# Kernel optimization log

Measured on AMD Instinct MI355X. Metric: run time of the kernel, lower is better.

## Reference

```python
import jax, jax.numpy as jnp
import numpy as np

P, L, E, D, NL, FF = 1024, 32, 512, 768, 6, 3072
H_PA, H_TR = 4, 8
VOCAB = 256


def layer_norm(x, w, b, eps=1e-5):
    mu = x.mean(-1, keepdims=True)
    var = ((x - mu) ** 2).mean(-1, keepdims=True)
    return (x - mu) / jnp.sqrt(var + eps) * w + b


def mha(x, wqkv, bqkv, wo, bo, nheads, key_mask=None):
    # x: [B,S,E]; torch nn.MultiheadAttention semantics (scale q by 1/sqrt(d))
    B, S, Emb = x.shape
    d = Emb // nheads
    qkv = x @ wqkv.T + bqkv
    q, k, v = jnp.split(qkv, 3, axis=-1)
    hd = lambda t: t.reshape(B, S, nheads, d).transpose(0, 2, 1, 3)
    q, k, v = hd(q) * (d ** -0.5), hd(k), hd(v)
    scores = jnp.einsum('bhqd,bhkd->bhqk', q, k)
    if key_mask is not None:
        scores = jnp.where(key_mask[:, None, None, :], scores, -1e9)
    a = jax.nn.softmax(scores, axis=-1)
    o = jnp.einsum('bhqk,bhkd->bhqd', a, v).transpose(0, 2, 1, 3).reshape(B, S, Emb)
    return o @ wo.T + bo


def setup_inputs() -> dict:
    key = jax.random.key(0)
    ks = jax.random.split(key, 32)
    n = lambda i, shape, s=0.02: (jax.random.normal(ks[i], shape, dtype=jnp.float32) * s)
    x = lambda i, shape: jax.random.normal(ks[i], shape, dtype=jnp.float32) * (1.0 / np.sqrt(shape[-1]))
    tokens = jax.random.randint(ks[0], (P, L), 0, VOCAB, dtype=jnp.int32)
    lengths = jax.random.randint(ks[1], (P,), 4, L + 1, dtype=jnp.int32)
    byte_emb = n(2, (VOCAB, E)).at[0].set(0.0)  # padding_idx=0
    inp = {
        'tokens': tokens, 'lengths': lengths,
        'byte_emb': byte_emb,
        'local_pos_emb': n(3, (L, E)),
        'patch_pos_emb': n(4, (P, D)),
        'pa_qkv_w': x(5, (3 * E, E)), 'pa_qkv_b': jnp.zeros((3 * E,), jnp.float32),
        'pa_out_w': x(6, (E, E)), 'pa_out_b': jnp.zeros((E,), jnp.float32),
        'proj_w': x(7, (D, E)), 'proj_b': jnp.zeros((D,), jnp.float32),
        'layers_qkv_w': x(8, (NL, 3 * D, D)), 'layers_qkv_b': jnp.zeros((NL, 3 * D), jnp.float32),
        'layers_out_w': x(9, (NL, D, D)), 'layers_out_b': jnp.zeros((NL, D), jnp.float32),
        'layers_ln1_w': jnp.ones((NL, D), jnp.float32), 'layers_ln1_b': jnp.zeros((NL, D), jnp.float32),
        'layers_ln2_w': jnp.ones((NL, D), jnp.float32), 'layers_ln2_b': jnp.zeros((NL, D), jnp.float32),
        'layers_ff1_w': x(10, (NL, FF, D)), 'layers_ff1_b': jnp.zeros((NL, FF), jnp.float32),
        'layers_ff2_w': x(11, (NL, D, FF)), 'layers_ff2_b': jnp.zeros((NL, D), jnp.float32),
        'ln_f_w': jnp.ones((D,), jnp.float32), 'ln_f_b': jnp.zeros((D,), jnp.float32),
    }
    return inp


def reference(tokens, lengths, byte_emb, local_pos_emb, patch_pos_emb,
              pa_qkv_w, pa_qkv_b, pa_out_w, pa_out_b, proj_w, proj_b,
              layers_qkv_w, layers_qkv_b, layers_out_w, layers_out_b,
              layers_ln1_w, layers_ln1_b, layers_ln2_w, layers_ln2_b,
              layers_ff1_w, layers_ff1_b, layers_ff2_w, layers_ff2_b,
              ln_f_w, ln_f_b):
    mask = jnp.arange(L) < lengths[:, None]  # [P,L] valid-byte mask
    # encode_patches: byte embed + local positions, zero padded slots
    emb = byte_emb[tokens] + local_pos_emb[None, :, :]  # [P,L,E]
    emb = emb * mask[..., None].astype(emb.dtype)
    # per-patch MHA over bytes (key padding mask), vectorized across patches
    attn = mha(emb, pa_qkv_w, pa_qkv_b, pa_out_w, pa_out_b, H_PA, key_mask=mask)
    cnt = mask.sum(-1, keepdims=True).astype(emb.dtype)
    patch_repr = (attn * mask[..., None].astype(emb.dtype)).sum(1) / cnt  # [P,E] masked mean
    # project to hidden and add patch-level positions
    h = patch_repr @ proj_w.T + proj_b + patch_pos_emb[:P]
    h = h[None]  # [1,P,D]
    # pre-norm transformer encoder, gelu FFN
    for i in range(NL):
        hn = layer_norm(h, layers_ln1_w[i], layers_ln1_b[i])
        h = h + mha(hn, layers_qkv_w[i], layers_qkv_b[i], layers_out_w[i], layers_out_b[i], H_TR)
        hn = layer_norm(h, layers_ln2_w[i], layers_ln2_b[i])
        ff = jax.nn.gelu(hn @ layers_ff1_w[i].T + layers_ff1_b[i], approximate=False)
        h = h + ff @ layers_ff2_w[i].T + layers_ff2_b[i]
    return layer_norm(h, ln_f_w, ln_f_b)[0]  # [P,D]
```

## Files before the change

kernel.cpp:

```cpp
#include <hip/hip_runtime.h>
#include <hip/hip_bf16.h>
#include <math.h>

typedef __hip_bfloat16 bf16;
typedef unsigned short u16;
typedef __attribute__((ext_vector_type(8))) short short8;
typedef __attribute__((ext_vector_type(4))) float f32x4;

#define PP 1024
#define LL 32
#define EE 512
#define DD 768
#define NLAYER 6
#define FFDIM 3072

__device__ __forceinline__ float bf2f(u16 u) { return __uint_as_float(((unsigned)u) << 16); }
__device__ __forceinline__ u16 f2b(float x) {
  unsigned u = __float_as_uint(x);
  return (u16)((u + 0x7FFFu + ((u >> 16) & 1u)) >> 16);
}

__global__ __launch_bounds__(256) void cvt4(
    const float* s0, const float* s1, const float* s2, const float* s3,
    u16* d0, u16* d1, u16* d2, u16* d3,
    int n0, int n1, int n2, int n3)
{
  int r = blockIdx.y;
  const float* s = r == 0 ? s0 : r == 1 ? s1 : r == 2 ? s2 : s3;
  u16* d        = r == 0 ? d0 : r == 1 ? d1 : r == 2 ? d2 : d3;
  int n4        = r == 0 ? n0 : r == 1 ? n1 : r == 2 ? n2 : n3;
  int i = blockIdx.x * 256 + threadIdx.x;
  if (i < n4) {
    float4 v = ((const float4*)s)[i];
    ushort4 o;
    o.x = f2b(v.x); o.y = f2b(v.y); o.z = f2b(v.z); o.w = f2b(v.w);
    ((ushort4*)d)[i] = o;
  }
}

__global__ __launch_bounds__(256) void embed_table(
    const float* __restrict__ be, const float* __restrict__ lp, bf16* __restrict__ T)
{
  int i = blockIdx.x * 256 + threadIdx.x;
  int r = i >> 6, c = (i & 63) << 3;
  int t = r >> 5, l = r & 31;
  const float* bp = be + ((long)t << 9) + c;
  const float* pp = lp + ((long)l << 9) + c;
  float4 x0 = *(const float4*)bp, x1 = *(const float4*)(bp + 4);
  float4 y0 = *(const float4*)pp, y1 = *(const float4*)(pp + 4);
  short8 o;
  o[0] = (short)f2b(x0.x + y0.x); o[1] = (short)f2b(x0.y + y0.y);
  o[2] = (short)f2b(x0.z + y0.z); o[3] = (short)f2b(x0.w + y0.w);
  o[4] = (short)f2b(x1.x + y1.x); o[5] = (short)f2b(x1.y + y1.y);
  o[6] = (short)f2b(x1.z + y1.z); o[7] = (short)f2b(x1.w + y1.w);
  *(short8*)((u16*)T + ((long)r << 9) + c) = o;
}

template<bool AEMB>
__global__ __launch_bounds__(256) void gemm64(
    const bf16* A, long sAb, int lda,
    const bf16* B, long sBb, int ldb,
    float* Cf, bf16* Cb, long sCb, int ldc,
    const float* bias, int biasStride,
    const float* addf,
    int M, int N, int K, int act,
    const int* tokens, const int* lengths,
    const float* be, const float* lp)
{
  __shared__ u16 As[2][64][72];
  __shared__ u16 Bs[2][64][72];
  const int bz = blockIdx.z;
  const u16* Ap = (const u16*)A + (long)bz * sAb;
  const u16* Bp = (const u16*)B + (long)bz * sBb;
  const long coff = (long)bz * sCb;
  const int m0 = blockIdx.x << 6, n0 = blockIdx.y << 6;
  const int tid = threadIdx.x;
  const int wave = tid >> 6, lane = tid & 63;
  const int sr = tid >> 3;
  const int scc = (tid & 7) << 3;
  const int br0 = n0 + sr, br1 = n0 + sr + 32;
  const short8 zz = {0,0,0,0,0,0,0,0};
  f32x4 acc[4] = {{0.f,0.f,0.f,0.f},{0.f,0.f,0.f,0.f},{0.f,0.f,0.f,0.f},{0.f,0.f,0.f,0.f}};

#define LOADA(row, kk, dest)                                                   \
  do {                                                                         \
    if (!AEMB) {                                                               \
      dest = *(const short8*)(Ap + (long)(row) * lda + (kk));                  \
    } else {                                                                   \
      int rr = (row); int ll = rr & 31;                                        \
      if (ll < lengths[rr >> 5]) {                                             \
        const float* bpp = be + ((long)tokens[rr] << 9) + (kk);                \
        const float* lpp = lp + ((long)ll << 9) + (kk);                        \
        float4 x0 = *(const float4*)bpp, x1 = *(const float4*)(bpp + 4);       \
        float4 y0 = *(const float4*)lpp, y1 = *(const float4*)(lpp + 4);       \
        dest[0] = (short)f2b(x0.x + y0.x); dest[1] = (short)f2b(x0.y + y0.y);  \
        dest[2] = (short)f2b(x0.z + y0.z); dest[3] = (short)f2b(x0.w + y0.w);  \
        dest[4] = (short)f2b(x1.x + y1.x); dest[5] = (short)f2b(x1.y + y1.y);  \
        dest[6] = (short)f2b(x1.z + y1.z); dest[7] = (short)f2b(x1.w + y1.w);  \
      } else dest = zz;                                                        \
    }                                                                          \
  } while (0)

  {
    int ch = K < 64 ? K : 64;
    bool kv = scc < ch;
    short8 a0 = zz, a1 = zz, b0 = zz, b1 = zz;
    if (kv) {
      LOADA(m0 + sr, scc, a0);
      LOADA(m0 + sr + 32, scc, a1);
      if (br0 < N) b0 = *(const short8*)(Bp + (long)br0 * ldb + scc);
      if (br1 < N) b1 = *(const short8*)(Bp + (long)br1 * ldb + scc);
    }
    *(short8*)&As[0][sr][scc] = a0;
    *(short8*)&As[0][sr + 32][scc] = a1;
    *(short8*)&Bs[0][sr][scc] = b0;
    *(short8*)&Bs[0][sr + 32][scc] = b1;
  }
  __syncthreads();

  const int arow = (wave << 4) + (lane & 15);
  const int kq = (lane >> 4) << 3;
  int buf = 0;
  for (int k0 = 0; k0 < K; k0 += 64) {
    int knext = k0 + 64;
    bool more = knext < K;
    short8 a0 = zz, a1 = zz, b0 = zz, b1 = zz;
    if (more) {
      int ch = K - knext; if (ch > 64) ch = 64;
      bool kv = scc < ch;
      if (kv) {
        LOADA(m0 + sr, knext + scc, a0);
        LOADA(m0 + sr + 32, knext + scc, a1);
        if (br0 < N) b0 = *(const short8*)(Bp + (long)br0 * ldb + knext + scc);
        if (br1 < N) b1 = *(const short8*)(Bp + (long)br1 * ldb + knext + scc);
      }
    }
    int rem = K - k0; if (rem > 64) rem = 64;
    {
      short8 af = *(const short8*)&As[buf][arow][kq];
#pragma unroll
      for (int nt = 0; nt < 4; nt++) {
        short8 bfr = *(const short8*)&Bs[buf][(nt << 4) + (lane & 15)][kq];
        acc[nt] = __builtin_amdgcn_mfma_f32_16x16x32_bf16(af, bfr, acc[nt], 0, 0, 0);
      }
    }
    if (rem > 32) {
      short8 af = *(const short8*)&As[buf][arow][32 + kq];
#pragma unroll
      for (int nt = 0; nt < 4; nt++) {
        short8 bfr = *(const short8*)&Bs[buf][(nt << 4) + (lane & 15)][32 + kq];
        acc[nt] = __builtin_amdgcn_mfma_f32_16x16x32_bf16(af, bfr, acc[nt], 0, 0, 0);
      }
    }
    if (more) {
      int nb = buf ^ 1;
      *(short8*)&As[nb][sr][scc] = a0;
      *(short8*)&As[nb][sr + 32][scc] = a1;
      *(short8*)&Bs[nb][sr][scc] = b0;
      *(short8*)&Bs[nb][sr + 32][scc] = b1;
      __syncthreads();
      buf = nb;
    }
  }
#undef LOADA

  int rbase = m0 + (wave << 4) + ((lane >> 4) << 2);
#pragma unroll
  for (int nt = 0; nt < 4; nt++) {
    int c = n0 + (nt << 4) + (lane & 15);
    if (c >= N) continue;
    float bvl = bias ? bias[bz * biasStride + c] : 0.f;
#pragma unroll
    for (int j = 0; j < 4; j++) {
      int r = rbase + j;
      long idx = coff + (long)r * ldc + c;
      float v = acc[nt][j] + bvl;
      if (addf) v += addf[idx];
      if (act == 1) v = 0.5f * v * (1.f + erff(v * 0.70710678118654752f));
      if (Cf) Cf[idx] = v;
      if (Cb) Cb[idx] = __float2bfloat16(v);
    }
  }
}

__global__ __launch_bounds__(256) void patch_attn(
    const bf16* __restrict__ qkt,
    const int* __restrict__ tokens, const int* __restrict__ lengths,
    const float* __restrict__ byte_emb, const float* __restrict__ local_pos,
    bf16* __restrict__ Z)
{
  __shared__ float wsum[4][32];
  __shared__ int tok_s[32];
  __shared__ int cnt_s;
  int p = blockIdx.x;
  int tid = threadIdx.x;
  if (tid < 32) tok_s[tid] = tokens[p * 32 + tid];
  if (tid == 0) cnt_s = lengths[p];
  __syncthreads();
  int cnt = cnt_s;
  int h = tid >> 6, lane = tid & 63;
  const int rsel = lane & 15;
  const int ksel = (lane >> 4) << 3;
  const u16* qkb = (const u16*)qkt + h * 128;
  const long r0 = ((long)((tok_s[rsel] << 5) | rsel)) << 10;
  const long r1 = ((long)((tok_s[16 + rsel] << 5) | (16 + rsel))) << 10;

  f32x4 acc[2][2] = {{{0.f,0.f,0.f,0.f},{0.f,0.f,0.f,0.f}},
                     {{0.f,0.f,0.f,0.f},{0.f,0.f,0.f,0.f}}};
#pragma unroll
  for (int kc = 0; kc < 4; kc++) {
    int ko = kc * 32 + ksel;
    short8 a0 = *(const short8*)(qkb + r0 + ko);
    short8 a1 = *(const short8*)(qkb + r1 + ko);
    short8 b0 = *(const short8*)(qkb + r0 + 512 + ko);
    short8 b1 = *(const short8*)(qkb + r1 + 512 + ko);
    acc[0][0] = __builtin_amdgcn_mfma_f32_16x16x32_bf16(a0, b0, acc[0][0], 0, 0, 0);
    acc[0][1] = __builtin_amdgcn_mfma_f32_16x16x32_bf16(a0, b1, acc[0][1], 0, 0, 0);
    acc[1][0] = __builtin_amdgcn_mfma_f32_16x16x32_bf16(a1, b0, acc[1][0], 0, 0, 0);
    acc[1][1] = __builtin_amdgcn_mfma_f32_16x16x32_bf16(a1, b1, acc[1][1], 0, 0, 0);
  }

  const float scale = 0.088388347648318447f;
  int j0 = lane & 15, j1 = 16 + j0;
  bool v0 = j0 < cnt, v1 = j1 < cnt;
  int rowq = (lane >> 4) << 2;
  float cs0 = 0.f, cs1 = 0.f;
#pragma unroll
  for (int ti = 0; ti < 2; ti++) {
    float s0[4], s1[4], mx[4], sm[4], e0[4], e1[4];
#pragma unroll
    for (int r = 0; r < 4; r++) {
      s0[r] = acc[ti][0][r] * scale;
      s1[r] = acc[ti][1][r] * scale;
      float a = v0 ? s0[r] : -1e30f;
      float b = v1 ? s1[r] : -1e30f;
      mx[r] = fmaxf(a, b);
    }
#pragma unroll
    for (int d = 1; d < 16; d <<= 1)
#pragma unroll
      for (int r = 0; r < 4; r++) mx[r] = fmaxf(mx[r], __shfl_xor(mx[r], d));
#pragma unroll
    for (int r = 0; r < 4; r++) {
      e0[r] = v0 ? __expf(s0[r] - mx[r]) : 0.f;
      e1[r] = v1 ? __expf(s1[r] - mx[r]) : 0.f;
      sm[r] = e0[r] + e1[r];
    }
#pragma unroll
    for (int d = 1; d < 16; d <<= 1)
#pragma unroll
      for (int r = 0; r < 4; r++) sm[r] += __shfl_xor(sm[r], d);
#pragma unroll
    for (int r = 0; r < 4; r++) {
      int row = ti * 16 + rowq + r;
      if (row < cnt) {
        float inv = 1.f / sm[r];
        cs0 += e0[r] * inv;
        cs1 += e1[r] * inv;
      }
    }
  }
  cs0 += __shfl_xor(cs0, 16); cs0 += __shfl_xor(cs0, 32);
  cs1 += __shfl_xor(cs1, 16); cs1 += __shfl_xor(cs1, 32);
  if (lane < 16) {
    float invc = 1.f / (float)cnt;
    wsum[h][lane] = cs0 * invc;
    wsum[h][16 + lane] = cs1 * invc;
  }
  __syncthreads();

  for (int e = tid; e < 512; e += 256) {
    float za0 = 0.f, za1 = 0.f, za2 = 0.f, za3 = 0.f;
    for (int j = 0; j < cnt; j++) {
      float ev = byte_emb[((long)tok_s[j] << 9) + e] + local_pos[((long)j << 9) + e];
      za0 += wsum[0][j] * ev;
      za1 += wsum[1][j] * ev;
      za2 += wsum[2][j] * ev;
      za3 += wsum[3][j] * ev;
    }
    long zb = (long)p * 2048;
    Z[zb + e]        = __float2bfloat16(za0);
    Z[zb + 512 + e]  = __float2bfloat16(za1);
    Z[zb + 1024 + e] = __float2bfloat16(za2);
    Z[zb + 1536 + e] = __float2bfloat16(za3);
  }
}

__global__ __launch_bounds__(256) void ln_kernel(
    const float* __restrict__ x, const float* __restrict__ w, const float* __restrict__ b,
    bf16* outb, float* outf, int N)
{
  __shared__ float red[8];
  __shared__ float mv[2];
  int row = blockIdx.x;
  const float* xr = x + (long)row * N;
  int tid = threadIdx.x, lane = tid & 63, wave = tid >> 6;
  float s = 0.f, s2 = 0.f;
  for (int c = tid; c < N; c += 256) { float v = xr[c]; s += v; s2 += v * v; }
  for (int o = 32; o; o >>= 1) { s += __shfl_down(s, o); s2 += __shfl_down(s2, o); }
  if (lane == 0) { red[wave] = s; red[4 + wave] = s2; }
  __syncthreads();
  if (tid == 0) {
    float ts = red[0] + red[1] + red[2] + red[3];
    float ts2 = red[4] + red[5] + red[6] + red[7];
    float mu = ts / N;
    float var = ts2 / N - mu * mu;
    mv[0] = mu; mv[1] = rsqrtf(var + 1e-5f);
  }
  __syncthreads();
  float mu = mv[0], rstd = mv[1];
  for (int c = tid; c < N; c += 256) {
    float v = (xr[c] - mu) * rstd * w[c] + b[c];
    if (outb) outb[(long)row * N + c] = __float2bfloat16(v);
    if (outf) outf[(long)row * N + c] = v;
  }
}

__global__ __launch_bounds__(256) void softmax_bf(u16* __restrict__ S)
{
  __shared__ float red[4], red2[4];
  long row = blockIdx.x;
  u16* sr = S + row * 1024;
  int tid = threadIdx.x, lane = tid & 63, wave = tid >> 6;
  const float scale = 0.10206207261596577f;
  ushort4 raw = *(const ushort4*)(sr + tid * 4);
  float v[4] = {bf2f(raw.x) * scale, bf2f(raw.y) * scale, bf2f(raw.z) * scale, bf2f(raw.w) * scale};
  float m = fmaxf(fmaxf(v[0], v[1]), fmaxf(v[2], v[3]));
  for (int o = 32; o; o >>= 1) m = fmaxf(m, __shfl_down(m, o));
  if (lane == 0) red[wave] = m;
  __syncthreads();
  m = fmaxf(fmaxf(red[0], red[1]), fmaxf(red[2], red[3]));
  float s = 0.f;
#pragma unroll
  for (int k = 0; k < 4; k++) { v[k] = __expf(v[k] - m); s += v[k]; }
  for (int o = 32; o; o >>= 1) s += __shfl_down(s, o);
  if (lane == 0) red2[wave] = s;
  __syncthreads();
  s = red2[0] + red2[1] + red2[2] + red2[3];
  float inv = 1.f / s;
  ushort4 o4;
  o4.x = f2b(v[0] * inv); o4.y = f2b(v[1] * inv); o4.z = f2b(v[2] * inv); o4.w = f2b(v[3] * inv);
  *(ushort4*)(sr + tid * 4) = o4;
}

__global__ __launch_bounds__(256) void transpose_v(
    const bf16* __restrict__ qkv, bf16* __restrict__ Vt)
{
  __shared__ u16 tile[32][33];
  int k0 = blockIdx.x << 5;
  int d0 = blockIdx.y << 5;
  int tx = threadIdx.x & 31, ty = threadIdx.x >> 5;
  const u16* q = (const u16*)qkv;
  for (int i = ty; i < 32; i += 8)
    tile[i][tx] = q[(long)(k0 + i) * 2304 + 1536 + d0 + tx];
  __syncthreads();
  u16* vt = (u16*)Vt;
  for (int i = ty; i < 32; i += 8)
    vt[(long)(d0 + i) * 1024 + k0 + tx] = tile[tx][i];
}

extern "C" void kernel_launch(void* const* d_in, const int* in_sizes, int n_in,
                              void* d_out, int out_size, void* d_ws, size_t ws_size,
                              hipStream_t stream)
{
  const int*   tokens    = (const int*)d_in[0];
  const int*   lengths   = (const int*)d_in[1];
  const float* byte_emb  = (const float*)d_in[2];
  const float* local_pos = (const float*)d_in[3];
  const float* patch_pos = (const float*)d_in[4];
  const float* pa_qkv_w  = (const float*)d_in[5];
  const float* pa_qkv_b  = (const float*)d_in[6];
  const float* pa_out_w  = (const float*)d_in[7];
  const float* pa_out_b  = (const float*)d_in[8];
  const float* proj_w    = (const float*)d_in[9];
  const float* proj_b    = (const float*)d_in[10];
  const float* Wqkv      = (const float*)d_in[11];
  const float* Bqkv      = (const float*)d_in[12];
  const float* Wout      = (const float*)d_in[13];
  const float* Bout      = (const float*)d_in[14];
  const float* ln1w      = (const float*)d_in[15];
  const float* ln1b      = (const float*)d_in[16];
  const float* ln2w      = (const float*)d_in[17];
  const float* ln2b      = (const float*)d_in[18];
  const float* W1        = (const float*)d_in[19];
  const float* B1        = (const float*)d_in[20];
  const float* W2        = (const float*)d_in[21];
  const float* B2        = (const float*)d_in[22];
  const float* lnfw      = (const float*)d_in[23];
  const float* lnfb      = (const float*)d_in[24];

  char* ws = (char*)d_ws;
  const size_t MB = 1ull << 20;
  bf16* qkT    = (bf16*)(ws);
  u16*  scores = (u16*)(ws);
  bf16* qkvt   = (bf16*)(ws + 16 * MB);
  bf16* Vt     = (bf16*)(ws + 21 * MB);
  bf16* attn   = (bf16*)(ws + 23 * MB);
  bf16* ffb    = (bf16*)(ws + 25 * MB);
  float* h     = (float*)(ws + 31 * MB);
  bf16* hn     = (bf16*)(ws + 34 * MB);
  u16*  Lw     = (u16*)(ws + 36 * MB);
  bf16* embT   = (bf16*)(ws + 50 * MB);
  bf16* Z      = (bf16*)(ws + 64 * MB);
  bf16* o_mean = (bf16*)(ws + 68 * MB);
  bf16* t1     = (bf16*)(ws + 69 * MB);
  u16*  P1w    = (u16*)(ws + 70 * MB);

  const long oLQKV = 0;
  const long oLOUT = 1769472;
  const long oLW1  = 2359296;
  const long oLW2  = 4718592;
  const long oPAQ  = 0;
  const long oPAO  = 786432;
  const long oPRJ  = 1048576;

  cvt4<<<dim3(768, 3), 256, 0, stream>>>(
      pa_qkv_w, pa_out_w, proj_w, nullptr,
      P1w + oPAQ, P1w + oPAO, P1w + oPRJ, nullptr,
      786432 / 4, 262144 / 4, 393216 / 4, 0);
  embed_table<<<2048, 256, 0, stream>>>(byte_emb, local_pos, embT);
  gemm64<false><<<dim3(128, 16, 1), 256, 0, stream>>>(
      embT, 0, EE, (bf16*)(P1w + oPAQ), 0, EE, nullptr, qkT, 0, 1024,
      pa_qkv_b, 0, nullptr, 8192, 1024, EE, 0,
      nullptr, nullptr, nullptr, nullptr);
  patch_attn<<<PP, 256, 0, stream>>>(
      qkT, tokens, lengths, byte_emb, local_pos, Z);
  gemm64<false><<<dim3(16, 2, 4), 256, 0, stream>>>(
      Z, 512, 2048, (bf16*)(P1w + oPAQ + 1024L * EE), 128L * EE, EE,
      nullptr, o_mean, 128, EE, pa_qkv_b + 1024, 128, nullptr, PP, 128, EE, 0,
      nullptr, nullptr, nullptr, nullptr);
  gemm64<false><<<dim3(16, 8, 1), 256, 0, stream>>>(
      o_mean, 0, EE, (bf16*)(P1w + oPAO), 0, EE, nullptr, t1, 0, EE,
      pa_out_b, 0, nullptr, PP, EE, EE, 0,
      nullptr, nullptr, nullptr, nullptr);
  gemm64<false><<<dim3(16, 12, 1), 256, 0, stream>>>(
      t1, 0, EE, (bf16*)(P1w + oPRJ), 0, EE, h, nullptr, 0, DD,
      proj_b, 0, patch_pos, PP, DD, EE, 0,
      nullptr, nullptr, nullptr, nullptr);

  for (int i = 0; i < NLAYER; i++) {
    cvt4<<<dim3(2304, 4), 256, 0, stream>>>(
        Wqkv + (long)i * 2304 * DD, Wout + (long)i * DD * DD,
        W1 + (long)i * FFDIM * DD, W2 + (long)i * DD * FFDIM,
        Lw + oLQKV, Lw + oLOUT, Lw + oLW1, Lw + oLW2,
        1769472 / 4, 589824 / 4, 2359296 / 4, 2359296 / 4);
    ln_kernel<<<PP, 256, 0, stream>>>(h, ln1w + i * DD, ln1b + i * DD, hn, nullptr, DD);
    gemm64<false><<<dim3(16, 36, 1), 256, 0, stream>>>(
        hn, 0, DD, (bf16*)(Lw + oLQKV), 0, DD, nullptr, qkvt, 0, 2304,
        Bqkv + i * 2304, 0, nullptr, PP, 2304, DD, 0,
        nullptr, nullptr, nullptr, nullptr);
    gemm64<false><<<dim3(16, 16, 8), 256, 0, stream>>>(
        qkvt, 96, 2304, qkvt + DD, 96, 2304, nullptr, (bf16*)scores, 1024L * 1024, 1024,
        nullptr, 0, nullptr, 1024, 1024, 96, 0,
        nullptr, nullptr, nullptr, nullptr);
    softmax_bf<<<8192, 256, 0, stream>>>(scores);
    transpose_v<<<dim3(32, 24), 256, 0, stream>>>(qkvt, Vt);
    gemm64<false><<<dim3(16, 2, 8), 256, 0, stream>>>(
        (bf16*)scores, 1024L * 1024, 1024, Vt, 96L * 1024, 1024, nullptr, attn, 96, DD,
        nullptr, 0, nullptr, 1024, 96, 1024, 0,
        nullptr, nullptr, nullptr, nullptr);
    gemm64<false><<<dim3(16, 12, 1), 256, 0, stream>>>(
        attn, 0, DD, (bf16*)(Lw + oLOUT), 0, DD, h, nullptr, 0, DD,
        Bout + i * DD, 0, h, PP, DD, DD, 0,
        nullptr, nullptr, nullptr, nullptr);
    ln_kernel<<<PP, 256, 0, stream>>>(h, ln2w + i * DD, ln2b + i * DD, hn, nullptr, DD);
    gemm64<false><<<dim3(16, 48, 1), 256, 0, stream>>>(
        hn, 0, DD, (bf16*)(Lw + oLW1), 0, DD, nullptr, ffb, 0, FFDIM,
        B1 + i * FFDIM, 0, nullptr, PP, FFDIM, DD, 1,
        nullptr, nullptr, nullptr, nullptr);
    gemm64<false><<<dim3(16, 12, 1), 256, 0, stream>>>(
        ffb, 0, FFDIM, (bf16*)(Lw + oLW2), 0, FFDIM, h, nullptr, 0, DD,
        B2 + i * DD, 0, h, PP, DD, FFDIM, 0,
        nullptr, nullptr, nullptr, nullptr);
  }
  ln_kernel<<<PP, 256, 0, stream>>>(h, lnfw, lnfb, nullptr, (float*)d_out, DD);
}
```

Baseline: 1.120 ms.

## Fuse fp32 weight conversion into GEMM loads and split-K residual GEMMs with atomics

Removes the separate per-layer fp32-to-bf16 weight conversion kernels and instead converts weights on the fly while loading B tiles in the GEMM. The out-projection and FF2 GEMMs are split along K across grid z, accumulating into the residual buffer with atomicAdd, with bias added only by the first split. This avoids the conversion kernels' write/read traffic and launches and increases block count for the narrow N=768 GEMMs. In exchange, GEMMs read 4-byte weights repeatedly per M-tile and the atomics make accumulation order nondeterministic.

```diff
diff --git a/kernel.cpp b/kernel.cpp
--- a/kernel.cpp
+++ b/kernel.cpp
@@ -18,24 +18,6 @@
 __device__ __forceinline__ u16 f2b(float x) {
   unsigned u = __float_as_uint(x);
   return (u16)((u + 0x7FFFu + ((u >> 16) & 1u)) >> 16);
-}
-
-__global__ __launch_bounds__(256) void cvt4(
-    const float* s0, const float* s1, const float* s2, const float* s3,
-    u16* d0, u16* d1, u16* d2, u16* d3,
-    int n0, int n1, int n2, int n3)
-{
-  int r = blockIdx.y;
-  const float* s = r == 0 ? s0 : r == 1 ? s1 : r == 2 ? s2 : s3;
-  u16* d        = r == 0 ? d0 : r == 1 ? d1 : r == 2 ? d2 : d3;
-  int n4        = r == 0 ? n0 : r == 1 ? n1 : r == 2 ? n2 : n3;
-  int i = blockIdx.x * 256 + threadIdx.x;
-  if (i < n4) {
-    float4 v = ((const float4*)s)[i];
-    ushort4 o;
-    o.x = f2b(v.x); o.y = f2b(v.y); o.z = f2b(v.z); o.w = f2b(v.w);
-    ((ushort4*)d)[i] = o;
-  }
 }
 
 __global__ __launch_bounds__(256) void embed_table(
@@ -56,22 +38,21 @@
   *(short8*)((u16*)T + ((long)r << 9) + c) = o;
 }
 
-template<bool AEMB>
+template<bool BF32>
 __global__ __launch_bounds__(256) void gemm64(
     const bf16* A, long sAb, int lda,
-    const bf16* B, long sBb, int ldb,
+    const void* B, long sBb, int ldb,
     float* Cf, bf16* Cb, long sCb, int ldc,
     const float* bias, int biasStride,
     const float* addf,
-    int M, int N, int K, int act,
-    const int* tokens, const int* lengths,
-    const float* be, const float* lp)
+    int M, int N, int K, int act)
 {
   __shared__ u16 As[2][64][72];
   __shared__ u16 Bs[2][64][72];
   const int bz = blockIdx.z;
   const u16* Ap = (const u16*)A + (long)bz * sAb;
   const u16* Bp = (const u16*)B + (long)bz * sBb;
+  const float* Bfp = (const float*)B + (long)bz * sBb;
   const long coff = (long)bz * sCb;
   const int m0 = blockIdx.x << 6, n0 = blockIdx.y << 6;
   const int tid = threadIdx.x;
@@ -82,22 +63,17 @@
   const short8 zz = {0,0,0,0,0,0,0,0};
   f32x4 acc[4] = {{0.f,0.f,0.f,0.f},{0.f,0.f,0.f,0.f},{0.f,0.f,0.f,0.f},{0.f,0.f,0.f,0.f}};
 
-#define LOADA(row, kk, dest)                                                   \
+#define LOADB(row, kk, dest)                                                   \
   do {                                                                         \
-    if (!AEMB) {                                                               \
-      dest = *(const short8*)(Ap + (long)(row) * lda + (kk));                  \
+    if (!BF32) {                                                               \
+      dest = *(const short8*)(Bp + (long)(row) * ldb + (kk));                  \
     } else {                                                                   \
-      int rr = (row); int ll = rr & 31;                                        \
-      if (ll < lengths[rr >> 5]) {                                             \
-        const float* bpp = be + ((long)tokens[rr] << 9) + (kk);                \
-        const float* lpp = lp + ((long)ll << 9) + (kk);                        \
-        float4 x0 = *(const float4*)bpp, x1 = *(const float4*)(bpp + 4);       \
-        float4 y0 = *(const float4*)lpp, y1 = *(const float4*)(lpp + 4);       \
-        dest[0] = (short)f2b(x0.x + y0.x); dest[1] = (short)f2b(x0.y + y0.y);  \
-        dest[2] = (short)f2b(x0.z + y0.z); dest[3] = (short)f2b(x0.w + y0.w);  \
-        dest[4] = (short)f2b(x1.x + y1.x); dest[5] = (short)f2b(x1.y + y1.y);  \
-        dest[6] = (short)f2b(x1.z + y1.z); dest[7] = (short)f2b(x1.w + y1.w);  \
-      } else dest = zz;                                                        \
+      const float* fp_ = Bfp + (long)(row) * ldb + (kk);                       \
+      float4 x0_ = *(const float4*)fp_, x1_ = *(const float4*)(fp_ + 4);       \
+      dest[0] = (short)f2b(x0_.x); dest[1] = (short)f2b(x0_.y);                \
+      dest[2] = (short)f2b(x0_.z); dest[3] = (short)f2b(x0_.w);                \
+      dest[4] = (short)f2b(x1_.x); dest[5] = (short)f2b(x1_.y);                \
+      dest[6] = (short)f2b(x1_.z); dest[7] = (short)f2b(x1_.w);                \
     }                                                                          \
   } while (0)
 
@@ -106,10 +82,10 @@
     bool kv = scc < ch;
     short8 a0 = zz, a1 = zz, b0 = zz, b1 = zz;
     if (kv) {
-      LOADA(m0 + sr, scc, a0);
-      LOADA(m0 + sr + 32, scc, a1);
-      if (br0 < N) b0 = *(const short8*)(Bp + (long)br0 * ldb + scc);
-      if (br1 < N) b1 = *(const short8*)(Bp + (long)br1 * ldb + scc);
+      a0 = *(const short8*)(Ap + (long)(m0 + sr) * lda + scc);
+      a1 = *(const short8*)(Ap + (long)(m0 + sr + 32) * lda + scc);
+      if (br0 < N) LOADB(br0, scc, b0);
+      if (br1 < N) LOADB(br1, scc, b1);
     }
     *(short8*)&As[0][sr][scc] = a0;
     *(short8*)&As[0][sr + 32][scc] = a1;
@@ -129,10 +105,10 @@
       int ch = K - knext; if (ch > 64) ch = 64;
       bool kv = scc < ch;
       if (kv) {
-        LOADA(m0 + sr, knext + scc, a0);
-        LOADA(m0 + sr + 32, knext + scc, a1);
-        if (br0 < N) b0 = *(const short8*)(Bp + (long)br0 * ldb + knext + scc);
-        if (br1 < N) b1 = *(const short8*)(Bp + (long)br1 * ldb + knext + scc);
+        a0 = *(const short8*)(Ap + (long)(m0 + sr) * lda + knext + scc);
+        a1 = *(const short8*)(Ap + (long)(m0 + sr + 32) * lda + knext + scc);
+        if (br0 < N) LOADB(br0, knext + scc, b0);
+        if (br1 < N) LOADB(br1, knext + scc, b1);
       }
     }
     int rem = K - k0; if (rem > 64) rem = 64;
@@ -162,7 +138,7 @@
       buf = nb;
     }
   }
-#undef LOADA
+#undef LOADB
 
   int rbase = m0 + (wave << 4) + ((lane >> 4) << 2);
 #pragma unroll
@@ -170,6 +146,7 @@
     int c = n0 + (nt << 4) + (lane & 15);
     if (c >= N) continue;
     float bvl = bias ? bias[bz * biasStride + c] : 0.f;
+    if (act == 2 && bz != 0) bvl = 0.f;
 #pragma unroll
     for (int j = 0; j < 4; j++) {
       int r = rbase + j;
@@ -177,8 +154,12 @@
       float v = acc[nt][j] + bvl;
       if (addf) v += addf[idx];
       if (act == 1) v = 0.5f * v * (1.f + erff(v * 0.70710678118654752f));
-      if (Cf) Cf[idx] = v;
-      if (Cb) Cb[idx] = __float2bfloat16(v);
+      if (act == 2) {
+        atomicAdd(Cf + idx, v);
+      } else {
+        if (Cf) Cf[idx] = v;
+        if (Cb) Cb[idx] = __float2bfloat16(v);
+      }
     }
   }
 }
@@ -399,79 +380,50 @@
   bf16* ffb    = (bf16*)(ws + 25 * MB);
   float* h     = (float*)(ws + 31 * MB);
   bf16* hn     = (bf16*)(ws + 34 * MB);
-  u16*  Lw     = (u16*)(ws + 36 * MB);
   bf16* embT   = (bf16*)(ws + 50 * MB);
   bf16* Z      = (bf16*)(ws + 64 * MB);
   bf16* o_mean = (bf16*)(ws + 68 * MB);
   bf16* t1     = (bf16*)(ws + 69 * MB);
-  u16*  P1w    = (u16*)(ws + 70 * MB);
-
-  const long oLQKV = 0;
-  const long oLOUT = 1769472;
-  const long oLW1  = 2359296;
-  const long oLW2  = 4718592;
-  const long oPAQ  = 0;
-  const long oPAO  = 786432;
-  const long oPRJ  = 1048576;
-
-  cvt4<<<dim3(768, 3), 256, 0, stream>>>(
-      pa_qkv_w, pa_out_w, proj_w, nullptr,
-      P1w + oPAQ, P1w + oPAO, P1w + oPRJ, nullptr,
-      786432 / 4, 262144 / 4, 393216 / 4, 0);
+
   embed_table<<<2048, 256, 0, stream>>>(byte_emb, local_pos, embT);
-  gemm64<false><<<dim3(128, 16, 1), 256, 0, stream>>>(
-      embT, 0, EE, (bf16*)(P1w + oPAQ), 0, EE, nullptr, qkT, 0, 1024,
-      pa_qkv_b, 0, nullptr, 8192, 1024, EE, 0,
-      nullptr, nullptr, nullptr, nullptr);
+  gemm64<true><<<dim3(128, 16, 1), 256, 0, stream>>>(
+      embT, 0, EE, pa_qkv_w, 0, EE, nullptr, qkT, 0, 1024,
+      pa_qkv_b, 0, nullptr, 8192, 1024, EE, 0);
   patch_attn<<<PP, 256, 0, stream>>>(
       qkT, tokens, lengths, byte_emb, local_pos, Z);
-  gemm64<false><<<dim3(16, 2, 4), 256, 0, stream>>>(
-      Z, 512, 2048, (bf16*)(P1w + oPAQ + 1024L * EE), 128L * EE, EE,
-      nullptr, o_mean, 128, EE, pa_qkv_b + 1024, 128, nullptr, PP, 128, EE, 0,
-      nullptr, nullptr, nullptr, nullptr);
-  gemm64<false><<<dim3(16, 8, 1), 256, 0, stream>>>(
-      o_mean, 0, EE, (bf16*)(P1w + oPAO), 0, EE, nullptr, t1, 0, EE,
-      pa_out_b, 0, nullptr, PP, EE, EE, 0,
-      nullptr, nullptr, nullptr, nullptr);
-  gemm64<false><<<dim3(16, 12, 1), 256, 0, stream>>>(
-      t1, 0, EE, (bf16*)(P1w + oPRJ), 0, EE, h, nullptr, 0, DD,
-      proj_b, 0, patch_pos, PP, DD, EE, 0,
-      nullptr, nullptr, nullptr, nullptr);
+  gemm64<true><<<dim3(16, 2, 4), 256, 0, stream>>>(
+      Z, 512, 2048, pa_qkv_w + 1024L * EE, 128L * EE, EE,
+      nullptr, o_mean, 128, EE, pa_qkv_b + 1024, 128, nullptr, PP, 128, EE, 0);
+  gemm64<true><<<dim3(16, 8, 1), 256, 0, stream>>>(
+      o_mean, 0, EE, pa_out_w, 0, EE, nullptr, t1, 0, EE,
+      pa_out_b, 0, nullptr, PP, EE, EE, 0);
+  gemm64<true><<<dim3(16, 12, 1), 256, 0, stream>>>(
+      t1, 0, EE, proj_w, 0, EE, h, nullptr, 0, DD,
+      proj_b, 0, patch_pos, PP, DD, EE, 0);
 
   for (int i = 0; i < NLAYER; i++) {
-    cvt4<<<dim3(2304, 4), 256, 0, stream>>>(
-        Wqkv + (long)i * 2304 * DD, Wout + (long)i * DD * DD,
-        W1 + (long)i * FFDIM * DD, W2 + (long)i * DD * FFDIM,
-        Lw + oLQKV, Lw + oLOUT, Lw + oLW1, Lw + oLW2,
-        1769472 / 4, 589824 / 4, 2359296 / 4, 2359296 / 4);
     ln_kernel<<<PP, 256, 0, stream>>>(h, ln1w + i * DD, ln1b + i * DD, hn, nullptr, DD);
-    gemm64<false><<<dim3(16, 36, 1), 256, 0, stream>>>(
-        hn, 0, DD, (bf16*)(Lw + oLQKV), 0, DD, nullptr, qkvt, 0, 2304,
-        Bqkv + i * 2304, 0, nullptr, PP, 2304, DD, 0,
-        nullptr, nullptr, nullptr, nullptr);
+    gemm64<true><<<dim3(16, 36, 1), 256, 0, stream>>>(
+        hn, 0, DD, Wqkv + (long)i * 2304 * DD, 0, DD, nullptr, qkvt, 0, 2304,
+        Bqkv + i * 2304, 0, nullptr, PP, 2304, DD, 0);
     gemm64<false><<<dim3(16, 16, 8), 256, 0, stream>>>(
         qkvt, 96, 2304, qkvt + DD, 96, 2304, nullptr, (bf16*)scores, 1024L * 1024, 1024,
-        nullptr, 0, nullptr, 1024, 1024, 96, 0,
-        nullptr, nullptr, nullptr, nullptr);
+        nullptr, 0, nullptr, 1024, 1024, 96, 0);
     softmax_bf<<<8192, 256, 0, stream>>>(scores);
     transpose_v<<<dim3(32, 24), 256, 0, stream>>>(qkvt, Vt);
     gemm64<false><<<dim3(16, 2, 8), 256, 0, stream>>>(
         (bf16*)scores, 1024L * 1024, 1024, Vt, 96L * 1024, 1024, nullptr, attn, 96, DD,
-        nullptr, 0, nullptr, 1024, 96, 1024, 0,
-        nullptr, nullptr, nullptr, nullptr);
-    gemm64<false><<<dim3(16, 12, 1), 256, 0, stream>>>(
-        attn, 0, DD, (bf16*)(Lw + oLOUT), 0, DD, h, nullptr, 0, DD,
-        Bout + i * DD, 0, h, PP, DD, DD, 0,
-        nullptr, nullptr, nullptr, nullptr);
+        nullptr, 0, nullptr, 1024, 96, 1024, 0);
+    gemm64<true><<<dim3(16, 12, 2), 256, 0, stream>>>(
+        attn, 384, DD, Wout + (long)i * DD * DD, 384, DD, h, nullptr, 0, DD,
+        Bout + i * DD, 0, nullptr, PP, DD, 384, 2);
     ln_kernel<<<PP, 256, 0, stream>>>(h, ln2w + i * DD, ln2b + i * DD, hn, nullptr, DD);
-    gemm64<false><<<dim3(16, 48, 1), 256, 0, stream>>>(
-        hn, 0, DD, (bf16*)(Lw + oLW1), 0, DD, nullptr, ffb, 0, FFDIM,
-        B1 + i * FFDIM, 0, nullptr, PP, FFDIM, DD, 1,
-        nullptr, nullptr, nullptr, nullptr);
-    gemm64<false><<<dim3(16, 12, 1), 256, 0, stream>>>(
-        ffb, 0, FFDIM, (bf16*)(Lw + oLW2), 0, FFDIM, h, nullptr, 0, DD,
-        B2 + i * DD, 0, h, PP, DD, FFDIM, 0,
-        nullptr, nullptr, nullptr, nullptr);
+    gemm64<true><<<dim3(16, 48, 1), 256, 0, stream>>>(
+        hn, 0, DD, W1 + (long)i * FFDIM * DD, 0, DD, nullptr, ffb, 0, FFDIM,
+        B1 + i * FFDIM, 0, nullptr, PP, FFDIM, DD, 1);
+    gemm64<true><<<dim3(16, 12, 4), 256, 0, stream>>>(
+        ffb, 768, FFDIM, W2 + (long)i * DD * FFDIM, 768, FFDIM, h, nullptr, 0, DD,
+        B2 + i * DD, 0, nullptr, PP, DD, 768, 2);
   }
   ln_kernel<<<PP, 256, 0, stream>>>(h, lnfw, lnfb, nullptr, (float*)d_out, DD);
 }
```

Result: slower. 1.228 ms (+9.6%).

## Split-K the out-proj and FF2 GEMMs with partial sums reduced in layernorm

Applied to the files above, without the earlier changes.

The out-projection and FF2 GEMMs, which had only 192 blocks on a long K, now run split-K with 2 and 4 partitions. Each partition writes fp32 partial results to a scratch buffer, and bias is applied only on the first partition. The next layernorm kernel now adds the residual and partials, writes back h, and normalizes, so the separate residual-add pass disappears. It also removes the unused embedding-gather template path from the GEMM. The cost is extra fp32 partial-buffer traffic in exchange for better CU occupancy.

```diff
diff --git a/kernel.cpp b/kernel.cpp
--- a/kernel.cpp
+++ b/kernel.cpp
@@ -56,16 +56,13 @@
   *(short8*)((u16*)T + ((long)r << 9) + c) = o;
 }
 
-template<bool AEMB>
 __global__ __launch_bounds__(256) void gemm64(
     const bf16* A, long sAb, int lda,
     const bf16* B, long sBb, int ldb,
     float* Cf, bf16* Cb, long sCb, int ldc,
     const float* bias, int biasStride,
     const float* addf,
-    int M, int N, int K, int act,
-    const int* tokens, const int* lengths,
-    const float* be, const float* lp)
+    int M, int N, int K, int act)
 {
   __shared__ u16 As[2][64][72];
   __shared__ u16 Bs[2][64][72];
@@ -82,32 +79,13 @@
   const short8 zz = {0,0,0,0,0,0,0,0};
   f32x4 acc[4] = {{0.f,0.f,0.f,0.f},{0.f,0.f,0.f,0.f},{0.f,0.f,0.f,0.f},{0.f,0.f,0.f,0.f}};
 
-#define LOADA(row, kk, dest)                                                   \
-  do {                                                                         \
-    if (!AEMB) {                                                               \
-      dest = *(const short8*)(Ap + (long)(row) * lda + (kk));                  \
-    } else {                                                                   \
-      int rr = (row); int ll = rr & 31;                                        \
-      if (ll < lengths[rr >> 5]) {                                             \
-        const float* bpp = be + ((long)tokens[rr] << 9) + (kk);                \
-        const float* lpp = lp + ((long)ll << 9) + (kk);                        \
-        float4 x0 = *(const float4*)bpp, x1 = *(const float4*)(bpp + 4);       \
-        float4 y0 = *(const float4*)lpp, y1 = *(const float4*)(lpp + 4);       \
-        dest[0] = (short)f2b(x0.x + y0.x); dest[1] = (short)f2b(x0.y + y0.y);  \
-        dest[2] = (short)f2b(x0.z + y0.z); dest[3] = (short)f2b(x0.w + y0.w);  \
-        dest[4] = (short)f2b(x1.x + y1.x); dest[5] = (short)f2b(x1.y + y1.y);  \
-        dest[6] = (short)f2b(x1.z + y1.z); dest[7] = (short)f2b(x1.w + y1.w);  \
-      } else dest = zz;                                                        \
-    }                                                                          \
-  } while (0)
-
   {
     int ch = K < 64 ? K : 64;
     bool kv = scc < ch;
     short8 a0 = zz, a1 = zz, b0 = zz, b1 = zz;
     if (kv) {
-      LOADA(m0 + sr, scc, a0);
-      LOADA(m0 + sr + 32, scc, a1);
+      a0 = *(const short8*)(Ap + (long)(m0 + sr) * lda + scc);
+      a1 = *(const short8*)(Ap + (long)(m0 + sr + 32) * lda + scc);
       if (br0 < N) b0 = *(const short8*)(Bp + (long)br0 * ldb + scc);
       if (br1 < N) b1 = *(const short8*)(Bp + (long)br1 * ldb + scc);
     }
@@ -129,8 +107,8 @@
       int ch = K - knext; if (ch > 64) ch = 64;
       bool kv = scc < ch;
       if (kv) {
-        LOADA(m0 + sr, knext + scc, a0);
-        LOADA(m0 + sr + 32, knext + scc, a1);
+        a0 = *(const short8*)(Ap + (long)(m0 + sr) * lda + knext + scc);
+        a1 = *(const short8*)(Ap + (long)(m0 + sr + 32) * lda + knext + scc);
         if (br0 < N) b0 = *(const short8*)(Bp + (long)br0 * ldb + knext + scc);
         if (br1 < N) b1 = *(const short8*)(Bp + (long)br1 * ldb + knext + scc);
       }
@@ -162,7 +140,6 @@
       buf = nb;
     }
   }
-#undef LOADA
 
   int rbase = m0 + (wave << 4) + ((lane >> 4) << 2);
 #pragma unroll
@@ -170,6 +147,7 @@
     int c = n0 + (nt << 4) + (lane & 15);
     if (c >= N) continue;
     float bvl = bias ? bias[bz * biasStride + c] : 0.f;
+    if (act == 2 && bz != 0) bvl = 0.f;
 #pragma unroll
     for (int j = 0; j < 4; j++) {
       int r = rbase + j;
@@ -287,32 +265,49 @@
 }
 
 __global__ __launch_bounds__(256) void ln_kernel(
-    const float* __restrict__ x, const float* __restrict__ w, const float* __restrict__ b,
-    bf16* outb, float* outf, int N)
+    const float* __restrict__ x,
+    const float* __restrict__ a0, const float* __restrict__ a1,
+    const float* __restrict__ a2, const float* __restrict__ a3,
+    float* __restrict__ hout,
+    const float* __restrict__ w, const float* __restrict__ b,
+    bf16* outb, float* outf)
 {
   __shared__ float red[8];
   __shared__ float mv[2];
   int row = blockIdx.x;
-  const float* xr = x + (long)row * N;
+  long base = (long)row * DD;
   int tid = threadIdx.x, lane = tid & 63, wave = tid >> 6;
+  float vv[3];
   float s = 0.f, s2 = 0.f;
-  for (int c = tid; c < N; c += 256) { float v = xr[c]; s += v; s2 += v * v; }
+#pragma unroll
+  for (int j = 0; j < 3; j++) {
+    long c = base + tid + j * 256;
+    float v = x[c];
+    if (a0) v += a0[c];
+    if (a1) v += a1[c];
+    if (a2) v += a2[c];
+    if (a3) v += a3[c];
+    if (hout) hout[c] = v;
+    vv[j] = v; s += v; s2 += v * v;
+  }
   for (int o = 32; o; o >>= 1) { s += __shfl_down(s, o); s2 += __shfl_down(s2, o); }
   if (lane == 0) { red[wave] = s; red[4 + wave] = s2; }
   __syncthreads();
   if (tid == 0) {
     float ts = red[0] + red[1] + red[2] + red[3];
     float ts2 = red[4] + red[5] + red[6] + red[7];
-    float mu = ts / N;
-    float var = ts2 / N - mu * mu;
+    float mu = ts / DD;
+    float var = ts2 / DD - mu * mu;
     mv[0] = mu; mv[1] = rsqrtf(var + 1e-5f);
   }
   __syncthreads();
   float mu = mv[0], rstd = mv[1];
-  for (int c = tid; c < N; c += 256) {
-    float v = (xr[c] - mu) * rstd * w[c] + b[c];
-    if (outb) outb[(long)row * N + c] = __float2bfloat16(v);
-    if (outf) outf[(long)row * N + c] = v;
+#pragma unroll
+  for (int j = 0; j < 3; j++) {
+    int c = tid + j * 256;
+    float v = (vv[j] - mu) * rstd * w[c] + b[c];
+    if (outb) outb[base + c] = __float2bfloat16(v);
+    if (outf) outf[base + c] = v;
   }
 }
 
@@ -401,10 +396,13 @@
   bf16* hn     = (bf16*)(ws + 34 * MB);
   u16*  Lw     = (u16*)(ws + 36 * MB);
   bf16* embT   = (bf16*)(ws + 50 * MB);
+  float* hp    = (float*)(ws + 58 * MB);
   bf16* Z      = (bf16*)(ws + 64 * MB);
   bf16* o_mean = (bf16*)(ws + 68 * MB);
   bf16* t1     = (bf16*)(ws + 69 * MB);
   u16*  P1w    = (u16*)(ws + 70 * MB);
+
+  const long PSTRIDE = (long)PP * DD;
 
   const long oLQKV = 0;
   const long oLOUT = 1769472;
@@ -419,24 +417,20 @@
       P1w + oPAQ, P1w + oPAO, P1w + oPRJ, nullptr,
       786432 / 4, 262144 / 4, 393216 / 4, 0);
   embed_table<<<2048, 256, 0, stream>>>(byte_emb, local_pos, embT);
-  gemm64<false><<<dim3(128, 16, 1), 256, 0, stream>>>(
+  gemm64<<<dim3(128, 16, 1), 256, 0, stream>>>(
       embT, 0, EE, (bf16*)(P1w + oPAQ), 0, EE, nullptr, qkT, 0, 1024,
-      pa_qkv_b, 0, nullptr, 8192, 1024, EE, 0,
-      nullptr, nullptr, nullptr, nullptr);
+      pa_qkv_b, 0, nullptr, 8192, 1024, EE, 0);
   patch_attn<<<PP, 256, 0, stream>>>(
       qkT, tokens, lengths, byte_emb, local_pos, Z);
-  gemm64<false><<<dim3(16, 2, 4), 256, 0, stream>>>(
+  gemm64<<<dim3(16, 2, 4), 256, 0, stream>>>(
       Z, 512, 2048, (bf16*)(P1w + oPAQ + 1024L * EE), 128L * EE, EE,
-      nullptr, o_mean, 128, EE, pa_qkv_b + 1024, 128, nullptr, PP, 128, EE, 0,
-      nullptr, nullptr, nullptr, nullptr);
-  gemm64<false><<<dim3(16, 8, 1), 256, 0, stream>>>(
+      nullptr, o_mean, 128, EE, pa_qkv_b + 1024, 128, nullptr, PP, 128, EE, 0);
+  gemm64<<<dim3(16, 8, 1), 256, 0, stream>>>(
       o_mean, 0, EE, (bf16*)(P1w + oPAO), 0, EE, nullptr, t1, 0, EE,
-      pa_out_b, 0, nullptr, PP, EE, EE, 0,
-      nullptr, nullptr, nullptr, nullptr);
-  gemm64<false><<<dim3(16, 12, 1), 256, 0, stream>>>(
+      pa_out_b, 0, nullptr, PP, EE, EE, 0);
+  gemm64<<<dim3(16, 12, 1), 256, 0, stream>>>(
       t1, 0, EE, (bf16*)(P1w + oPRJ), 0, EE, h, nullptr, 0, DD,
-      proj_b, 0, patch_pos, PP, DD, EE, 0,
-      nullptr, nullptr, nullptr, nullptr);
+      proj_b, 0, patch_pos, PP, DD, EE, 0);
 
   for (int i = 0; i < NLAYER; i++) {
     cvt4<<<dim3(2304, 4), 256, 0, stream>>>(
@@ -444,34 +438,35 @@
         W1 + (long)i * FFDIM * DD, W2 + (long)i * DD * FFDIM,
         Lw + oLQKV, Lw + oLOUT, Lw + oLW1, Lw + oLW2,
         1769472 / 4, 589824 / 4, 2359296 / 4, 2359296 / 4);
-    ln_kernel<<<PP, 256, 0, stream>>>(h, ln1w + i * DD, ln1b + i * DD, hn, nullptr, DD);
-    gemm64<false><<<dim3(16, 36, 1), 256, 0, stream>>>(
+    if (i == 0)
+      ln_kernel<<<PP, 256, 0, stream>>>(h, nullptr, nullptr, nullptr, nullptr,
+                                        nullptr, ln1w + i * DD, ln1b + i * DD, hn, nullptr);
+    else
+      ln_kernel<<<PP, 256, 0, stream>>>(h, hp, hp + PSTRIDE, hp + 2 * PSTRIDE, hp + 3 * PSTRIDE,
+                                        h, ln1w + i * DD, ln1b + i * DD, hn, nullptr);
+    gemm64<<<dim3(16, 36, 1), 256, 0, stream>>>(
         hn, 0, DD, (bf16*)(Lw + oLQKV), 0, DD, nullptr, qkvt, 0, 2304,
-        Bqkv + i * 2304, 0, nullptr, PP, 2304, DD, 0,
-        nullptr, nullptr, nullptr, nullptr);
-    gemm64<false><<<dim3(16, 16, 8), 256, 0, stream>>>(
+        Bqkv + i * 2304, 0, nullptr, PP, 2304, DD, 0);
+    gemm64<<<dim3(16, 16, 8), 256, 0, stream>>>(
         qkvt, 96, 2304, qkvt + DD, 96, 2304, nullptr, (bf16*)scores, 1024L * 1024, 1024,
-        nullptr, 0, nullptr, 1024, 1024, 96, 0,
-        nullptr, nullptr, nullptr, nullptr);
+        nullptr, 0, nullptr, 1024, 1024, 96, 0);
     softmax_bf<<<8192, 256, 0, stream>>>(scores);
     transpose_v<<<dim3(32, 24), 256, 0, stream>>>(qkvt, Vt);
-    gemm64<false><<<dim3(16, 2, 8), 256, 0, stream>>>(
+    gemm64<<<dim3(16, 2, 8), 256, 0, stream>>>(
         (bf16*)scores, 1024L * 1024, 1024, Vt, 96L * 1024, 1024, nullptr, attn, 96, DD,
-        nullptr, 0, nullptr, 1024, 96, 1024, 0,
-        nullptr, nullptr, nullptr, nullptr);
-    gemm64<false><<<dim3(16, 12, 1), 256, 0, stream>>>(
-        attn, 0, DD, (bf16*)(Lw + oLOUT), 0, DD, h, nullptr, 0, DD,
-        Bout + i * DD, 0, h, PP, DD, DD, 0,
-        nullptr, nullptr, nullptr, nullptr);
-    ln_kernel<<<PP, 256, 0, stream>>>(h, ln2w + i * DD, ln2b + i * DD, hn, nullptr, DD);
-    gemm64<false><<<dim3(16, 48, 1), 256, 0, stream>>>(
+        nullptr, 0, nullptr, 1024, 96, 1024, 0);
+    gemm64<<<dim3(16, 12, 2), 256, 0, stream>>>(
+        attn, 384, DD, (bf16*)(Lw + oLOUT), 384, DD, hp, nullptr, PSTRIDE, DD,
+        Bout + i * DD, 0, nullptr, PP, DD, 384, 2);
+    ln_kernel<<<PP, 256, 0, stream>>>(h, hp, hp + PSTRIDE, nullptr, nullptr,
+                                      h, ln2w + i * DD, ln2b + i * DD, hn, nullptr);
+    gemm64<<<dim3(16, 48, 1), 256, 0, stream>>>(
         hn, 0, DD, (bf16*)(Lw + oLW1), 0, DD, nullptr, ffb, 0, FFDIM,
-        B1 + i * FFDIM, 0, nullptr, PP, FFDIM, DD, 1,
-        nullptr, nullptr, nullptr, nullptr);
-    gemm64<false><<<dim3(16, 12, 1), 256, 0, stream>>>(
-        ffb, 0, FFDIM, (bf16*)(Lw + oLW2), 0, FFDIM, h, nullptr, 0, DD,
-        B2 + i * DD, 0, h, PP, DD, FFDIM, 0,
-        nullptr, nullptr, nullptr, nullptr);
-  }
-  ln_kernel<<<PP, 256, 0, stream>>>(h, lnfw, lnfb, nullptr, (float*)d_out, DD);
-}
+        B1 + i * FFDIM, 0, nullptr, PP, FFDIM, DD, 1);
+    gemm64<<<dim3(16, 12, 4), 256, 0, stream>>>(
+        ffb, 768, FFDIM, (bf16*)(Lw + oLW2), 768, FFDIM, hp, nullptr, PSTRIDE, DD,
+        B2 + i * DD, 0, nullptr, PP, DD, 768, 2);
+  }
+  ln_kernel<<<PP, 256, 0, stream>>>(h, hp, hp + PSTRIDE, hp + 2 * PSTRIDE, hp + 3 * PSTRIDE,
+                                    nullptr, lnfw, lnfb, nullptr, (float*)d_out);
+}
```

Measured after the change: 988.6 us. -11.7%, faster.
